# Kernel optimization log

Measured on AMD Instinct MI355X. Metric: run time of the kernel, lower is better.

The kernel has to match this reference:

```python
import jax, jax.numpy as jnp
import numpy as np

R = 0.9        # ball-query radius
K = 32         # max neighbors per ball
STRIDE = 4     # spatial stride -> M = N // STRIDE reference points
EPS = 1e-5     # BatchNorm eps


def fps(xyz, m):
    """Furthest point sampling (pointnet2 semantics: start at index 0).
    xyz: (N,3) -> (m,) int32 indices."""
    N = xyz.shape[0]

    def step(carry, _):
        dist, last = carry
        d = jnp.sum((xyz - xyz[last]) ** 2, axis=-1)
        dist = jnp.minimum(dist, d)
        nxt = jnp.argmax(dist).astype(jnp.int32)
        return (dist, nxt), nxt

    init = (jnp.full((N,), 1e10, dtype=xyz.dtype), jnp.int32(0))
    _, rest = jax.lax.scan(step, init, None, length=m - 1)
    return jnp.concatenate([jnp.zeros((1,), jnp.int32), rest])


def sample_group(xyz):
    """FPS + ball query + grouping for one frame. xyz: (N,3).
    Returns ref (M,3), disp4 (M,K,4)."""
    N = xyz.shape[0]
    m = N // STRIDE
    fi = fps(xyz, m)
    ref = xyz[fi]                                              # (M,3)
    d2 = jnp.sum((ref[:, None, :] - xyz[None, :, :]) ** 2, -1)  # (M,N)
    # pointnet2 ball_query: first K in-radius indices (original order),
    # positions without a neighbor padded with the first found index.
    cand = jnp.where(d2 < R * R, jnp.arange(N, dtype=jnp.int32)[None, :], N)
    idx = jnp.sort(cand, axis=1)[:, :K]                        # (M,K)
    idx = jnp.where(idx == N, idx[:, :1], idx)
    nb = xyz[idx]                                              # (M,K,3)
    disp = nb - ref[:, None, :]
    disp4 = jnp.concatenate([disp, jnp.zeros_like(disp[..., :1])], axis=-1)
    return ref, disp4


def batch_norm(h, gamma, beta):
    # torch BN (training-mode) per frame: stats over (B, M, K) per t.
    # h: (B,T,M,K,C)
    mean = jnp.mean(h, axis=(0, 2, 3), keepdims=True)
    var = jnp.mean((h - mean) ** 2, axis=(0, 2, 3), keepdims=True)
    return gamma * (h - mean) * jax.lax.rsqrt(var + EPS) + beta


def setup_inputs() -> dict:
    key = jax.random.key(0)
    ks = jax.random.split(key, 7)
    B, T, N = 2, 8, 4096
    C1, C2 = 64, 128
    return {
        "xyzs": jax.random.normal(ks[0], (B, T, N, 3), dtype=jnp.float32),
        "W1": jax.random.normal(ks[1], (C1, 4), dtype=jnp.float32) * 0.1,
        "g1": jnp.ones((C1,), jnp.float32),
        "b1": jnp.zeros((C1,), jnp.float32),
        "W2": jax.random.normal(ks[2], (C2, C1), dtype=jnp.float32) * 0.1,
        "g2": jnp.ones((C2,), jnp.float32),
        "b2": jnp.zeros((C2,), jnp.float32),
    }


def reference(xyzs, W1, g1, b1, W2, g2, b2):
    # xyzs: (B,T,N,3)
    ref, disp4 = jax.vmap(jax.vmap(sample_group))(xyzs)  # (B,T,M,3), (B,T,M,K,4)
    h = jnp.einsum('btmkc,oc->btmko', disp4, W1)         # conv_d 1x1
    h = jax.nn.relu(batch_norm(h, g1, b1))
    h = jnp.einsum('btmkc,oc->btmko', h, W2)             # mlp 1x1
    h = jax.nn.relu(batch_norm(h, g2, b2))
    feat = jnp.max(h, axis=3)                            # max over K -> (B,T,M,C)
    new_features = jnp.transpose(feat, (0, 1, 3, 2))     # (B,T,C,M) like torch
    return ref, new_features
```

## Files before the change

### kernel.cpp

```cpp
#include <hip/hip_runtime.h>
#include <hip/hip_bf16.h>


#define N_PTS   4096
#define M_PTS   1024
#define KNB     32

typedef _Float16 half8 __attribute__((ext_vector_type(8)));
typedef float    f32x4 __attribute__((ext_vector_type(4)));

__device__ inline float2 pk_sub(float2 a, float2 b) {
  float2 d;
  asm("v_pk_add_f32 %0, %1, %2 neg_lo:[0,1] neg_hi:[0,1]" : "=v"(d) : "v"(a), "v"(b));
  return d;
}
__device__ inline float2 pk_mul(float2 a, float2 b) {
  float2 d;
  asm("v_pk_mul_f32 %0, %1, %2" : "=v"(d) : "v"(a), "v"(b));
  return d;
}
__device__ inline float2 pk_add(float2 a, float2 b) {
  float2 d;
  asm("v_pk_add_f32 %0, %1, %2" : "=v"(d) : "v"(a), "v"(b));
  return d;
}

#define DPPMAXF(ctrl)                                                          \
  {                                                                            \
    unsigned _o = (unsigned)__builtin_amdgcn_update_dpp(                       \
        0, (int)__float_as_uint(m), (ctrl), 0xF, 0xF, true);                   \
    m = fmaxf(m, __uint_as_float(_o));                                         \
  }

__device__ inline float4 fold1_chan(const float* __restrict__ acc9, int t, int c,
                                    const float* __restrict__ W1,
                                    const float* __restrict__ g1,
                                    const float* __restrict__ b1) {
  const float inv_n = 1.0f / 65536.0f;
  const float* a = acc9 + t * 9;
  float mx = a[0] * inv_n, my = a[1] * inv_n, mz = a[2] * inv_n;
  float Sxx = a[3] * inv_n, Syy = a[4] * inv_n, Szz = a[5] * inv_n;
  float Sxy = a[6] * inv_n, Sxz = a[7] * inv_n, Syz = a[8] * inv_n;
  float w0 = W1[c * 4], w1 = W1[c * 4 + 1], w2 = W1[c * 4 + 2];
  float mean = w0 * mx + w1 * my + w2 * mz;
  float E2 = w0 * w0 * Sxx + w1 * w1 * Syy + w2 * w2 * Szz
           + 2.f * (w0 * w1 * Sxy + w0 * w2 * Sxz + w1 * w2 * Syz);
  float var = E2 - mean * mean;
  float al = g1[c] / sqrtf(var + 1e-5f);
  float4 o; o.x = w0 * al; o.y = w1 * al; o.z = w2 * al; o.w = b1[c] - mean * al;
  return o;
}

__global__ __launch_bounds__(512) void fps_kernel(const float* __restrict__ xyzs,
                                                  float* __restrict__ out) {
#pragma clang fp contract(off)
  const int bt  = blockIdx.x & 15;
  const int tid = threadIdx.x;
  __shared__ float sx[N_PTS], syy[N_PTS], szz[N_PTS];
  __shared__ __align__(16) unsigned swp[2][16];
  __shared__ int sidx[M_PTS];

  const float* f = xyzs + (size_t)bt * (N_PTS * 3);
  for (int i = tid; i < N_PTS; i += 512) {
    sx[i]  = f[3 * i + 0];
    syy[i] = f[3 * i + 1];
    szz[i] = f[3 * i + 2];
  }
  if (tid == 0) sidx[0] = 0;
  __syncthreads();

  const int base = tid << 3;
  float2 px2[4], py2[4], pz2[4], dd2[4];
#pragma unroll
  for (int j = 0; j < 4; ++j) {
    int i0 = base + 2 * j;
    px2[j] = {sx[i0], sx[i0 + 1]};
    py2[j] = {syy[i0], syy[i0 + 1]};
    pz2[j] = {szz[i0], szz[i0 + 1]};
    dd2[j] = {1e10f, 1e10f};
  }
  float wx = sx[0], wy = syy[0], wz = szz[0];

  for (int it = 1; it < M_PTS; ++it) {
    float2 wxx = {wx, wx}, wyy = {wy, wy}, wzz = {wz, wz};
#pragma unroll
    for (int j = 0; j < 4; ++j) {
      float2 dx = pk_sub(px2[j], wxx);
      float2 dy = pk_sub(py2[j], wyy);
      float2 dz = pk_sub(pz2[j], wzz);
      float2 m1 = pk_mul(dx, dx);
      float2 m2 = pk_mul(dy, dy);
      float2 s  = pk_add(m1, m2);
      float2 m3 = pk_mul(dz, dz);
      float2 dt = pk_add(s, m3);
      dd2[j].x = fminf(dd2[j].x, dt.x);
      dd2[j].y = fminf(dd2[j].y, dt.y);
    }
    float v4[4]; int s4[4];
#pragma unroll
    for (int a = 0; a < 4; ++a) {
      bool t = dd2[a].y > dd2[a].x;
      v4[a] = t ? dd2[a].y : dd2[a].x;
      s4[a] = 2 * a + (t ? 1 : 0);
    }
    float v2[2]; int s2v[2];
#pragma unroll
    for (int a = 0; a < 2; ++a) {
      bool t = v4[2 * a + 1] > v4[2 * a];
      v2[a] = t ? v4[2 * a + 1] : v4[2 * a];
      s2v[a] = t ? s4[2 * a + 1] : s4[2 * a];
    }
    bool t1 = v2[1] > v2[0];
    float bv = t1 ? v2[1] : v2[0];
    int   bj = t1 ? s2v[1] : s2v[0];

    float m = bv;
    DPPMAXF(0x111);
    DPPMAXF(0x112);
    DPPMAXF(0x114);
    DPPMAXF(0x118);
    DPPMAXF(0x142);
    DPPMAXF(0x143);
    float vmax = __uint_as_float(
        (unsigned)__builtin_amdgcn_readlane((int)__float_as_uint(m), 63));
    bool match = (bv == vmax);
    unsigned long long mk = __ballot(match);
    int wl  = __builtin_ctzll(mk);
    int bjw = __builtin_amdgcn_readlane(bj, wl);
    const int w = tid >> 6;
    unsigned gi = (unsigned)((((w << 6) + wl) << 3) + bjw);

    const int p = it & 1;
    if ((tid & 63) == 63) {
      swp[p][2 * w]     = __float_as_uint(vmax);
      swp[p][2 * w + 1] = gi;
    }
    __syncthreads();
    uint4 A  = *(const uint4*)&swp[p][0];
    uint4 Bq = *(const uint4*)&swp[p][4];
    uint4 Cq = *(const uint4*)&swp[p][8];
    uint4 Dq = *(const uint4*)&swp[p][12];
    unsigned va, ga, vb, gb, vc, gc, vd, gd;
    { bool t = A.z  > A.x;  va = t ? A.z  : A.x;  ga = t ? A.w  : A.y;  }
    { bool t = Bq.z > Bq.x; vb = t ? Bq.z : Bq.x; gb = t ? Bq.w : Bq.y; }
    { bool t = Cq.z > Cq.x; vc = t ? Cq.z : Cq.x; gc = t ? Cq.w : Cq.y; }
    { bool t = Dq.z > Dq.x; vd = t ? Dq.z : Dq.x; gd = t ? Dq.w : Dq.y; }
    { bool t = vb > va; va = t ? vb : va; ga = t ? gb : ga; }
    { bool t = vd > vc; vc = t ? vd : vc; gc = t ? gd : gc; }
    { bool t = vc > va; va = t ? vc : va; ga = t ? gc : ga; }
    int bi = (int)ga;
    wx = sx[bi]; wy = syy[bi]; wz = szz[bi];
    if (tid == 0) sidx[it] = bi;
  }
  __syncthreads();
  float* orow = out + (size_t)bt * (M_PTS * 3);
  for (int i = tid; i < M_PTS; i += 512) {
    int ix = sidx[i];
    orow[3 * i + 0] = sx[ix];
    orow[3 * i + 1] = syy[ix];
    orow[3 * i + 2] = szz[ix];
  }
}

__global__ __launch_bounds__(256) void ball_kernel(const float* __restrict__ xyzs,
                                                   const float* __restrict__ refpts,
                                                   float* __restrict__ disp4) {
#pragma clang fp contract(off)
  const int lane = threadIdx.x & 63;
  const int gw   = (blockIdx.x << 2) + (threadIdx.x >> 6);
  const int bt   = gw >> 10;
  const float* f = xyzs + (size_t)bt * (N_PTS * 3);
  const float* r = refpts + (size_t)gw * 3;
  const float rx = r[0], ry = r[1], rz = r[2];
  float* dout = disp4 + (size_t)gw * (KNB * 4);

  int filled = 0;
  float p0x = 0.f, p0y = 0.f, p0z = 0.f;
  bool got0 = false;

  for (int base = 0; base < N_PTS; base += 64) {
    if (filled >= KNB) break;
    int j = base + lane;
    float x = f[3 * j], y = f[3 * j + 1], z = f[3 * j + 2];
    float dx = rx - x, dy = ry - y, dz = rz - z;
    float d2 = (dx * dx + dy * dy) + dz * dz;
    bool pred = d2 < 0.81f;
    unsigned long long mk = __ballot(pred);
    if (!got0 && mk) {
      int src = __builtin_ctzll(mk);
      p0x = __shfl(-dx, src); p0y = __shfl(-dy, src); p0z = __shfl(-dz, src);
      got0 = true;
    }
    int slot = filled + __popcll(mk & ((1ull << lane) - 1));
    if (pred && slot < KNB) {
      float4 v; v.x = -dx; v.y = -dy; v.z = -dz; v.w = 0.f;
      *(float4*)(dout + slot * 4) = v;
    }
    filled += __popcll(mk);
  }
  if (filled < KNB) {
    for (int s = filled + lane; s < KNB; s += 64) {
      float4 v; v.x = p0x; v.y = p0y; v.z = p0z; v.w = 0.f;
      *(float4*)(dout + s * 4) = v;
    }
  }
}

__global__ __launch_bounds__(256) void stats1_kernel(const float* __restrict__ disp4,
                                                     float* __restrict__ acc) {
  const int t = blockIdx.x >> 5, chunk = blockIdx.x & 31;
  const int tid = threadIdx.x;
  float s[9];
#pragma unroll
  for (int q = 0; q < 9; ++q) s[q] = 0.f;
  for (int i = tid; i < 2048; i += 256) {
    int smp = (chunk << 11) + i;
    size_t flat = ((size_t)(smp >> 15) << 18) + ((size_t)t << 15) + (smp & 32767);
    float4 v = ((const float4*)disp4)[flat];
    s[0] += v.x;       s[1] += v.y;       s[2] += v.z;
    s[3] += v.x * v.x; s[4] += v.y * v.y; s[5] += v.z * v.z;
    s[6] += v.x * v.y; s[7] += v.x * v.z; s[8] += v.y * v.z;
  }
#pragma unroll
  for (int q = 0; q < 9; ++q) {
#pragma unroll
    for (int off = 1; off < 64; off <<= 1) s[q] += __shfl_xor(s[q], off);
  }
  if ((tid & 63) == 0) {
    float* a = acc + t * 9;
#pragma unroll
    for (int q = 0; q < 9; ++q) atomicAdd(&a[q], s[q]);
  }
}

__global__ __launch_bounds__(256) void gram_kernel(const float* __restrict__ disp4,
                                                   const float* __restrict__ acc9,
                                                   const float* __restrict__ W1,
                                                   const float* __restrict__ g1,
                                                   const float* __restrict__ b1,
                                                   float* __restrict__ sumy,
                                                   float* __restrict__ G) {
  const int t = blockIdx.x >> 5, chunk = blockIdx.x & 31;
  const int tid = threadIdx.x;
  __shared__ float4 sdisp[32];
  __shared__ float  yt[32][64];
  __shared__ float  red[256];

  const int c = tid & 63, s0 = tid >> 6;
  float4 wc = fold1_chan(acc9, t, c, W1, g1, b1);
  const int r0 = (tid >> 4) << 2, q0 = (tid & 15) << 2;
  float acc[16];
#pragma unroll
  for (int q = 0; q < 16; ++q) acc[q] = 0.f;
  float ysum = 0.f;

  for (int b = 0; b < 64; ++b) {
    int sb = (chunk << 11) + (b << 5);
    if (tid < 32) {
      int smp = sb + tid;
      size_t flat = ((size_t)(smp >> 15) << 18) + ((size_t)t << 15) + (smp & 32767);
      sdisp[tid] = ((const float4*)disp4)[flat];
    }
    __syncthreads();
#pragma unroll
    for (int u = 0; u < 8; ++u) {
      int s = s0 * 8 + u;
      float4 d = sdisp[s];
      float y = wc.x * d.x + wc.y * d.y + wc.z * d.z + wc.w;
      y = y > 0.f ? y : 0.f;
      yt[s][c] = y;
      ysum += y;
    }
    __syncthreads();
#pragma unroll
    for (int s = 0; s < 32; ++s) {
      float4 av = *(const float4*)&yt[s][r0];
      float4 bv = *(const float4*)&yt[s][q0];
      acc[0]  += av.x * bv.x; acc[1]  += av.x * bv.y; acc[2]  += av.x * bv.z; acc[3]  += av.x * bv.w;
      acc[4]  += av.y * bv.x; acc[5]  += av.y * bv.y; acc[6]  += av.y * bv.z; acc[7]  += av.y * bv.w;
      acc[8]  += av.z * bv.x; acc[9]  += av.z * bv.y; acc[10] += av.z * bv.z; acc[11] += av.z * bv.w;
      acc[12] += av.w * bv.x; acc[13] += av.w * bv.y; acc[14] += av.w * bv.z; acc[15] += av.w * bv.w;
    }
    __syncthreads();
  }
  red[tid] = ysum;
  __syncthreads();
  if (tid < 64) {
    float v = red[tid] + red[tid + 64] + red[tid + 128] + red[tid + 192];
    atomicAdd(&sumy[t * 64 + tid], v);
  }
  float* Gp = G + t * 4096;
#pragma unroll
  for (int i = 0; i < 4; ++i)
#pragma unroll
    for (int j2 = 0; j2 < 4; ++j2)
      atomicAdd(&Gp[(r0 + i) * 64 + q0 + j2], acc[i * 4 + j2]);
}

__global__ __launch_bounds__(256) void fold2_kernel(const float* __restrict__ G,
    const float* __restrict__ sumy, const float* __restrict__ W2,
    const float* __restrict__ g2, const float* __restrict__ b2,
    _Float16* __restrict__ w2ph, float* __restrict__ beta2) {
  const int gidx = blockIdx.x * 256 + threadIdx.x;
  const int t = gidx >> 7, c2 = gidx & 127;
  const float inv_n = 1.f / 65536.f;
  const float* w = W2 + c2 * 64;
  float wreg[64];
#pragma unroll
  for (int q = 0; q < 16; ++q) {
    float4 v = ((const float4*)w)[q];
    wreg[4 * q] = v.x; wreg[4 * q + 1] = v.y; wreg[4 * q + 2] = v.z; wreg[4 * q + 3] = v.w;
  }
  float mean2 = 0.f;
#pragma unroll
  for (int j = 0; j < 64; ++j) mean2 += wreg[j] * (sumy[t * 64 + j] * inv_n);
  const float* Gp = G + t * 4096;
  float E2 = 0.f;
  for (int i = 0; i < 64; ++i) {
    const float* gr = Gp + i * 64;
    float gw = 0.f;
#pragma unroll
    for (int j = 0; j < 64; j += 4) {
      float4 gv = *(const float4*)&gr[j];
      gw += gv.x * wreg[j] + gv.y * wreg[j + 1] + gv.z * wreg[j + 2] + gv.w * wreg[j + 3];
    }
    E2 += wreg[i] * gw;
  }
  E2 *= inv_n;
  float var = E2 - mean2 * mean2;
  float al = g2[c2] / sqrtf(var + 1e-5f);
  float be = b2[c2] - mean2 * al;
  beta2[t * 128 + c2] = be;
  _Float16* wo = w2ph + (size_t)(t * 128 + c2) * 64;
#pragma unroll
  for (int j = 0; j < 64; ++j) wo[j] = (_Float16)(al * wreg[j]);
}

__global__ __launch_bounds__(256) void final_mfma(
    const float* __restrict__ disp4, const float* __restrict__ acc9,
    const float* __restrict__ W1, const float* __restrict__ g1,
    const float* __restrict__ b1,
    const _Float16* __restrict__ w2ph, const float* __restrict__ beta2,
    float* __restrict__ outfeat) {
  const int bid = blockIdx.x;
  const int bt = bid >> 6, mg = bid & 63;
  const int t = bt & 7;
  const int tid = threadIdx.x;
  const int lane = tid & 63, w = tid >> 6;

  __shared__ float4    sdisp[512];
  __shared__ _Float16  sy[512 * 64];

  {
    const float4* src = (const float4*)disp4 + (((size_t)(bt << 10) + (mg << 4)) << 5);
    sdisp[tid] = src[tid];
    sdisp[tid + 256] = src[tid + 256];
  }
  const int c0 = (tid & 31) * 2;
  float4 w1a = fold1_chan(acc9, t, c0, W1, g1, b1);
  float4 w1b = fold1_chan(acc9, t, c0 + 1, W1, g1, b1);
  __syncthreads();

  {
    const int r0 = (tid >> 5) * 64;
    const int hg = c0 >> 3;
    const int cin = (c0 & 7) * 2;
#pragma unroll 4
    for (int rr = 0; rr < 64; ++rr) {
      int row = r0 + rr;
      float4 d = sdisp[row];
      float ya = fmaxf(w1a.x * d.x + w1a.y * d.y + w1a.z * d.z + w1a.w, 0.f);
      float yb = fmaxf(w1b.x * d.x + w1b.y * d.y + w1b.z * d.z + w1b.w, 0.f);
      _Float16* p = (_Float16*)((char*)sy + row * 128 + ((hg ^ (row & 7)) * 16) + cin);
      p[0] = (_Float16)ya;
      p[1] = (_Float16)yb;
    }
  }
  __syncthreads();

  const int col = lane & 15, kg = lane >> 4;
  for (int ct = 0; ct < 8; ++ct) {
    const _Float16* wb = w2ph + ((size_t)(t * 128 + ct * 16 + col)) * 64 + kg * 8;
    half8 bf0 = *(const half8*)wb;
    half8 bf1 = *(const half8*)(wb + 32);
    float b2v = beta2[t * 128 + ct * 16 + col];
#pragma unroll
    for (int mi = 0; mi < 4; ++mi) {
      float mx = -1e30f;
#pragma unroll
      for (int h = 0; h < 2; ++h) {
        int row = (8 * w + 2 * mi + h) * 16 + col;
        int rm = row & 7;
        const char* rb = (const char*)sy + row * 128;
        half8 a0 = *(const half8*)(rb + ((kg ^ rm) * 16));
        half8 a1 = *(const half8*)(rb + (((4 + kg) ^ rm) * 16));
        f32x4 acc = {0.f, 0.f, 0.f, 0.f};
        acc = __builtin_amdgcn_mfma_f32_16x16x32_f16(a0, bf0, acc, 0, 0, 0);
        acc = __builtin_amdgcn_mfma_f32_16x16x32_f16(a1, bf1, acc, 0, 0, 0);
        float z = fmaxf(fmaxf(acc[0], acc[1]), fmaxf(acc[2], acc[3]));
        mx = fmaxf(mx, z);
      }
      mx = fmaxf(mx, __shfl_xor(mx, 16));
      mx = fmaxf(mx, __shfl_xor(mx, 32));
      if (lane < 16) {
        float v = fmaxf(mx + b2v, 0.f);
        int m = (mg << 4) + 4 * w + mi;
        outfeat[((size_t)(bt * 128 + ct * 16 + lane)) * 1024 + m] = v;
      }
    }
  }
}

extern "C" void kernel_launch(void* const* d_in, const int* in_sizes, int n_in,
                              void* d_out, int out_size, void* d_ws, size_t ws_size,
                              hipStream_t stream) {
  const float* xyzs = (const float*)d_in[0];
  const float* W1   = (const float*)d_in[1];
  const float* g1   = (const float*)d_in[2];
  const float* b1   = (const float*)d_in[3];
  const float* W2   = (const float*)d_in[4];
  const float* g2   = (const float*)d_in[5];
  const float* b2   = (const float*)d_in[6];
  float* out = (float*)d_out;
  float* ws  = (float*)d_ws;

  float*     disp4 = ws;
  float*     acc   = ws + 2097152;
  float*     sumy  = ws + 2097224;
  float*     G     = ws + 2097736;
  _Float16*  w2ph  = (_Float16*)(ws + 2130504);
  float*     beta2 = ws + 2163272;

  hipMemsetAsync(acc, 0, (72 + 512 + 32768) * sizeof(float), stream);
  fps_kernel   <<<256,  512, 0, stream>>>(xyzs, out);
  ball_kernel  <<<4096, 256, 0, stream>>>(xyzs, out, disp4);
  stats1_kernel<<<256,  256, 0, stream>>>(disp4, acc);
  gram_kernel  <<<256,  256, 0, stream>>>(disp4, acc, W1, g1, b1, sumy, G);
  fold2_kernel <<<4,    256, 0, stream>>>(G, sumy, W2, g2, b2, w2ph, beta2);
  final_mfma   <<<1024, 256, 0, stream>>>(disp4, acc, W1, g1, b1, w2ph, beta2, out + 49152);
}
```

Measured before the change: 1.124 ms.

## Fuse BN1 stats into ball query, MFMA gram, atomic argmax in FPS

FPS now reduces each iteration's argmax with a single 64-bit LDS atomicMax on a packed (iteration, value, inverted index) key, replacing the per-wave slot writes and the cross-wave compare tree. The ball-query kernel also accumulates the first-layer BatchNorm moment sums, so the separate stats pass over disp4 is removed. The gram kernel computes the 64x64 activation Gram matrix with fp16 MFMA instead of scalar fp32 FMAs. Together these aim to shorten the FPS serial loop, cut one full read of disp4, and speed up the gram step. The cost is fp16 rounding in the gram statistics and LDS atomic contention on ties.

```diff
diff --git a/kernel.cpp b/kernel.cpp
--- a/kernel.cpp
+++ b/kernel.cpp
@@ -57,7 +57,7 @@
   const int bt  = blockIdx.x & 15;
   const int tid = threadIdx.x;
   __shared__ float sx[N_PTS], syy[N_PTS], szz[N_PTS];
-  __shared__ __align__(16) unsigned swp[2][16];
+  __shared__ unsigned long long sslot[2];
   __shared__ int sidx[M_PTS];
 
   const float* f = xyzs + (size_t)bt * (N_PTS * 3);
@@ -66,7 +66,7 @@
     syy[i] = f[3 * i + 1];
     szz[i] = f[3 * i + 2];
   }
-  if (tid == 0) sidx[0] = 0;
+  if (tid == 0) { sidx[0] = 0; sslot[0] = 0ull; sslot[1] = 0ull; }
   __syncthreads();
 
   const int base = tid << 3;
@@ -123,32 +123,17 @@
     DPPMAXF(0x143);
     float vmax = __uint_as_float(
         (unsigned)__builtin_amdgcn_readlane((int)__float_as_uint(m), 63));
-    bool match = (bv == vmax);
-    unsigned long long mk = __ballot(match);
-    int wl  = __builtin_ctzll(mk);
-    int bjw = __builtin_amdgcn_readlane(bj, wl);
-    const int w = tid >> 6;
-    unsigned gi = (unsigned)((((w << 6) + wl) << 3) + bjw);
 
     const int p = it & 1;
-    if ((tid & 63) == 63) {
-      swp[p][2 * w]     = __float_as_uint(vmax);
-      swp[p][2 * w + 1] = gi;
+    if (bv == vmax) {
+      unsigned long long key = ((unsigned long long)(unsigned)it << 44)
+          | ((unsigned long long)__float_as_uint(bv) << 12)
+          | (unsigned long long)(4095u - (unsigned)((tid << 3) + bj));
+      atomicMax(&sslot[p], key);
     }
     __syncthreads();
-    uint4 A  = *(const uint4*)&swp[p][0];
-    uint4 Bq = *(const uint4*)&swp[p][4];
-    uint4 Cq = *(const uint4*)&swp[p][8];
-    uint4 Dq = *(const uint4*)&swp[p][12];
-    unsigned va, ga, vb, gb, vc, gc, vd, gd;
-    { bool t = A.z  > A.x;  va = t ? A.z  : A.x;  ga = t ? A.w  : A.y;  }
-    { bool t = Bq.z > Bq.x; vb = t ? Bq.z : Bq.x; gb = t ? Bq.w : Bq.y; }
-    { bool t = Cq.z > Cq.x; vc = t ? Cq.z : Cq.x; gc = t ? Cq.w : Cq.y; }
-    { bool t = Dq.z > Dq.x; vd = t ? Dq.z : Dq.x; gd = t ? Dq.w : Dq.y; }
-    { bool t = vb > va; va = t ? vb : va; ga = t ? gb : ga; }
-    { bool t = vd > vc; vc = t ? vd : vc; gc = t ? gd : gc; }
-    { bool t = vc > va; va = t ? vc : va; ga = t ? gc : ga; }
-    int bi = (int)ga;
+    unsigned long long kk = sslot[p];
+    int bi = 4095 - (int)(kk & 0xFFFull);
     wx = sx[bi]; wy = syy[bi]; wz = szz[bi];
     if (tid == 0) sidx[it] = bi;
   }
@@ -162,17 +147,24 @@
   }
 }
 
-__global__ __launch_bounds__(256) void ball_kernel(const float* __restrict__ xyzs,
-                                                   const float* __restrict__ refpts,
-                                                   float* __restrict__ disp4) {
+__global__ __launch_bounds__(256) void ball_stats(const float* __restrict__ xyzs,
+                                                  const float* __restrict__ refpts,
+                                                  float* __restrict__ disp4,
+                                                  float* __restrict__ acc9) {
 #pragma clang fp contract(off)
-  const int lane = threadIdx.x & 63;
-  const int gw   = (blockIdx.x << 2) + (threadIdx.x >> 6);
+  const int tid  = threadIdx.x;
+  const int lane = tid & 63, w = tid >> 6;
+  const int gw   = (blockIdx.x << 2) + w;
   const int bt   = gw >> 10;
   const float* f = xyzs + (size_t)bt * (N_PTS * 3);
   const float* r = refpts + (size_t)gw * 3;
   const float rx = r[0], ry = r[1], rz = r[2];
   float* dout = disp4 + (size_t)gw * (KNB * 4);
+  __shared__ float sred[4][9];
+
+  float st[9];
+#pragma unroll
+  for (int q = 0; q < 9; ++q) st[q] = 0.f;
 
   int filled = 0;
   float p0x = 0.f, p0y = 0.f, p0z = 0.f;
@@ -193,8 +185,12 @@
     }
     int slot = filled + __popcll(mk & ((1ull << lane) - 1));
     if (pred && slot < KNB) {
-      float4 v; v.x = -dx; v.y = -dy; v.z = -dz; v.w = 0.f;
+      float vx = -dx, vy = -dy, vz = -dz;
+      float4 v; v.x = vx; v.y = vy; v.z = vz; v.w = 0.f;
       *(float4*)(dout + slot * 4) = v;
+      st[0] += vx;      st[1] += vy;      st[2] += vz;
+      st[3] += vx * vx; st[4] += vy * vy; st[5] += vz * vz;
+      st[6] += vx * vy; st[7] += vx * vz; st[8] += vy * vz;
     }
     filled += __popcll(mk);
   }
@@ -203,56 +199,52 @@
       float4 v; v.x = p0x; v.y = p0y; v.z = p0z; v.w = 0.f;
       *(float4*)(dout + s * 4) = v;
     }
-  }
-}
-
-__global__ __launch_bounds__(256) void stats1_kernel(const float* __restrict__ disp4,
-                                                     float* __restrict__ acc) {
+    if (lane == 0) {
+      float cf = (float)(KNB - filled);
+      st[0] += cf * p0x;       st[1] += cf * p0y;       st[2] += cf * p0z;
+      st[3] += cf * p0x * p0x; st[4] += cf * p0y * p0y; st[5] += cf * p0z * p0z;
+      st[6] += cf * p0x * p0y; st[7] += cf * p0x * p0z; st[8] += cf * p0y * p0z;
+    }
+  }
+#pragma unroll
+  for (int q = 0; q < 9; ++q) {
+#pragma unroll
+    for (int off = 1; off < 64; off <<= 1) st[q] += __shfl_xor(st[q], off);
+  }
+  if (lane == 0) {
+#pragma unroll
+    for (int q = 0; q < 9; ++q) sred[w][q] = st[q];
+  }
+  __syncthreads();
+  if (tid < 9) {
+    float v = sred[0][tid] + sred[1][tid] + sred[2][tid] + sred[3][tid];
+    atomicAdd(&acc9[(bt & 7) * 9 + tid], v);
+  }
+}
+
+__global__ __launch_bounds__(256) void gram_mfma(
+    const float* __restrict__ disp4, const float* __restrict__ acc9,
+    const float* __restrict__ W1, const float* __restrict__ g1,
+    const float* __restrict__ b1,
+    float* __restrict__ sumy, float* __restrict__ G) {
   const int t = blockIdx.x >> 5, chunk = blockIdx.x & 31;
   const int tid = threadIdx.x;
-  float s[9];
-#pragma unroll
-  for (int q = 0; q < 9; ++q) s[q] = 0.f;
-  for (int i = tid; i < 2048; i += 256) {
-    int smp = (chunk << 11) + i;
-    size_t flat = ((size_t)(smp >> 15) << 18) + ((size_t)t << 15) + (smp & 32767);
-    float4 v = ((const float4*)disp4)[flat];
-    s[0] += v.x;       s[1] += v.y;       s[2] += v.z;
-    s[3] += v.x * v.x; s[4] += v.y * v.y; s[5] += v.z * v.z;
-    s[6] += v.x * v.y; s[7] += v.x * v.z; s[8] += v.y * v.z;
-  }
-#pragma unroll
-  for (int q = 0; q < 9; ++q) {
-#pragma unroll
-    for (int off = 1; off < 64; off <<= 1) s[q] += __shfl_xor(s[q], off);
-  }
-  if ((tid & 63) == 0) {
-    float* a = acc + t * 9;
-#pragma unroll
-    for (int q = 0; q < 9; ++q) atomicAdd(&a[q], s[q]);
-  }
-}
-
-__global__ __launch_bounds__(256) void gram_kernel(const float* __restrict__ disp4,
-                                                   const float* __restrict__ acc9,
-                                                   const float* __restrict__ W1,
-                                                   const float* __restrict__ g1,
-                                                   const float* __restrict__ b1,
-                                                   float* __restrict__ sumy,
-                                                   float* __restrict__ G) {
-  const int t = blockIdx.x >> 5, chunk = blockIdx.x & 31;
-  const int tid = threadIdx.x;
-  __shared__ float4 sdisp[32];
-  __shared__ float  yt[32][64];
-  __shared__ float  red[256];
-
-  const int c = tid & 63, s0 = tid >> 6;
+  const int lane = tid & 63, w = tid >> 6;
+  __shared__ float4    sdisp[32];
+  __shared__ _Float16  yt[2048];
+  __shared__ float     red[256];
+
+  const int c = lane;
   float4 wc = fold1_chan(acc9, t, c, W1, g1, b1);
-  const int r0 = (tid >> 4) << 2, q0 = (tid & 15) << 2;
-  float acc[16];
-#pragma unroll
-  for (int q = 0; q < 16; ++q) acc[q] = 0.f;
+  const int wswz = w ^ (c & 3) ^ ((c >> 2) & 3) ^ ((c >> 4) & 3);
+  _Float16* wp = (_Float16*)((char*)yt + c * 64 + wswz * 16);
+
+  f32x4 g0 = {0.f,0.f,0.f,0.f}, g1a = {0.f,0.f,0.f,0.f};
+  f32x4 g2a = {0.f,0.f,0.f,0.f}, g3 = {0.f,0.f,0.f,0.f};
   float ysum = 0.f;
+
+  const int frc = lane & 15, kg = lane >> 4;
+  const int fsw = kg ^ (lane & 3) ^ ((lane >> 2) & 3);
 
   for (int b = 0; b < 64; ++b) {
     int sb = (chunk << 11) + (b << 5);
@@ -262,25 +254,26 @@
       sdisp[tid] = ((const float4*)disp4)[flat];
     }
     __syncthreads();
+    half8 hv;
 #pragma unroll
     for (int u = 0; u < 8; ++u) {
-      int s = s0 * 8 + u;
-      float4 d = sdisp[s];
+      float4 d = sdisp[w * 8 + u];
       float y = wc.x * d.x + wc.y * d.y + wc.z * d.z + wc.w;
       y = y > 0.f ? y : 0.f;
-      yt[s][c] = y;
       ysum += y;
-    }
+      hv[u] = (_Float16)y;
+    }
+    *(half8*)wp = hv;
     __syncthreads();
-#pragma unroll
-    for (int s = 0; s < 32; ++s) {
-      float4 av = *(const float4*)&yt[s][r0];
-      float4 bv = *(const float4*)&yt[s][q0];
-      acc[0]  += av.x * bv.x; acc[1]  += av.x * bv.y; acc[2]  += av.x * bv.z; acc[3]  += av.x * bv.w;
-      acc[4]  += av.y * bv.x; acc[5]  += av.y * bv.y; acc[6]  += av.y * bv.z; acc[7]  += av.y * bv.w;
-      acc[8]  += av.z * bv.x; acc[9]  += av.z * bv.y; acc[10] += av.z * bv.z; acc[11] += av.z * bv.w;
-      acc[12] += av.w * bv.x; acc[13] += av.w * bv.y; acc[14] += av.w * bv.z; acc[15] += av.w * bv.w;
-    }
+    half8 fA = *(const half8*)((const char*)yt + (16 * w + frc) * 64 + ((fsw ^ w) * 16));
+    half8 f0 = *(const half8*)((const char*)yt + (frc) * 64       + ((fsw ^ 0) * 16));
+    half8 f1 = *(const half8*)((const char*)yt + (16 + frc) * 64  + ((fsw ^ 1) * 16));
+    half8 f2 = *(const half8*)((const char*)yt + (32 + frc) * 64  + ((fsw ^ 2) * 16));
+    half8 f3 = *(const half8*)((const char*)yt + (48 + frc) * 64  + ((fsw ^ 3) * 16));
+    g0  = __builtin_amdgcn_mfma_f32_16x16x32_f16(fA, f0, g0, 0, 0, 0);
+    g1a = __builtin_amdgcn_mfma_f32_16x16x32_f16(fA, f1, g1a, 0, 0, 0);
+    g2a = __builtin_amdgcn_mfma_f32_16x16x32_f16(fA, f2, g2a, 0, 0, 0);
+    g3  = __builtin_amdgcn_mfma_f32_16x16x32_f16(fA, f3, g3, 0, 0, 0);
     __syncthreads();
   }
   red[tid] = ysum;
@@ -290,11 +283,14 @@
     atomicAdd(&sumy[t * 64 + tid], v);
   }
   float* Gp = G + t * 4096;
-#pragma unroll
-  for (int i = 0; i < 4; ++i)
-#pragma unroll
-    for (int j2 = 0; j2 < 4; ++j2)
-      atomicAdd(&Gp[(r0 + i) * 64 + q0 + j2], acc[i * 4 + j2]);
+  const int rbase = 16 * w + (lane >> 4) * 4, cb = lane & 15;
+#pragma unroll
+  for (int r2 = 0; r2 < 4; ++r2) {
+    atomicAdd(&Gp[(rbase + r2) * 64 + cb],      g0[r2]);
+    atomicAdd(&Gp[(rbase + r2) * 64 + 16 + cb], g1a[r2]);
+    atomicAdd(&Gp[(rbase + r2) * 64 + 32 + cb], g2a[r2]);
+    atomicAdd(&Gp[(rbase + r2) * 64 + 48 + cb], g3[r2]);
+  }
 }
 
 __global__ __launch_bounds__(256) void fold2_kernel(const float* __restrict__ G,
@@ -432,10 +428,9 @@
   float*     beta2 = ws + 2163272;
 
   hipMemsetAsync(acc, 0, (72 + 512 + 32768) * sizeof(float), stream);
-  fps_kernel   <<<256,  512, 0, stream>>>(xyzs, out);
-  ball_kernel  <<<4096, 256, 0, stream>>>(xyzs, out, disp4);
-  stats1_kernel<<<256,  256, 0, stream>>>(disp4, acc);
-  gram_kernel  <<<256,  256, 0, stream>>>(disp4, acc, W1, g1, b1, sumy, G);
-  fold2_kernel <<<4,    256, 0, stream>>>(G, sumy, W2, g2, b2, w2ph, beta2);
-  final_mfma   <<<1024, 256, 0, stream>>>(disp4, acc, W1, g1, b1, w2ph, beta2, out + 49152);
-}
+  fps_kernel  <<<256,  512, 0, stream>>>(xyzs, out);
+  ball_stats  <<<4096, 256, 0, stream>>>(xyzs, out, disp4, acc);
+  gram_mfma   <<<256,  256, 0, stream>>>(disp4, acc, W1, g1, b1, sumy, G);
+  fold2_kernel<<<4,    256, 0, stream>>>(G, sumy, W2, g2, b2, w2ph, beta2);
+  final_mfma  <<<1024, 256, 0, stream>>>(disp4, acc, W1, g1, b1, w2ph, beta2, out + 49152);
+}
```

Result: faster. 996.0 us (-11.4%).
